# Kernel optimization log

Hardware: AMD Instinct MI355X
Metric: run time of the kernel (lower is better)

## Reference

```python
import jax, jax.numpy as jnp
import numpy as np


def setup_inputs() -> dict:
    key = jax.random.key(0)
    k1, k2, k3, k4, k5 = jax.random.split(key, 5)
    d_in, d_out, r = 1024, 1024, 32
    x = jax.random.normal(k1, (8, 8192, d_in), dtype=jnp.float32)
    W = jax.random.normal(k2, (d_out, d_in), dtype=jnp.float32) * (1.0 / np.sqrt(d_in))
    b = jax.random.normal(k3, (d_out,), dtype=jnp.float32) * 0.01
    V_r = jax.random.normal(k4, (d_in, r), dtype=jnp.float32) * (1.0 / np.sqrt(d_in))
    C = jax.random.normal(k5, (d_out, r), dtype=jnp.float32) * (1.0 / np.sqrt(r))
    return {"x": x, "W": W, "b": b, "V_r": V_r, "C": C}


def reference(x, W, b, V_r, C):
    # base = x @ W.T + b  (the quantized linear, modeled in fp32)
    base = jnp.einsum('bsd,od->bso', x, W) + b
    # low-rank correction: (x @ V_r) @ C.T  -- keep factored form, never
    # materialize the dense d_in x d_out correction matrix
    correction = jnp.einsum('bsr,or->bso', jnp.einsum('bsd,dr->bsr', x, V_r), C)
    return base + correction
```

## Files before the change

kernel.cpp:

```cpp
#include <hip/hip_runtime.h>
#include <hip/hip_bf16.h>

typedef __bf16 bf16_t;
typedef __bf16 bf16x8 __attribute__((ext_vector_type(8)));
typedef float  f32x4  __attribute__((ext_vector_type(4)));

#define DK 1024
#define DN 1024
#define RNK 32
#define BM 128
#define BN 256
#define BK 32
#define NKT 32

__global__ void weff_kernel(const float* __restrict__ W,
                            const float* __restrict__ Vr,
                            const float* __restrict__ C,
                            bf16_t* __restrict__ WeffSw)
{
    const int o  = blockIdx.x;
    const int g  = threadIdx.x;
    const int d0 = g * 8;

    f32x4 cv[8];
#pragma unroll
    for (int q = 0; q < 8; ++q) cv[q] = *(const f32x4*)(C + o * RNK + q * 4);

    const f32x4* wrow = (const f32x4*)(W + (size_t)o * DK + d0);
    f32x4 w0 = wrow[0], w1 = wrow[1];
    float acc[8];
#pragma unroll
    for (int e = 0; e < 4; ++e) { acc[e] = w0[e]; acc[4 + e] = w1[e]; }

#pragma unroll
    for (int e = 0; e < 8; ++e) {
        const f32x4* vre = (const f32x4*)(Vr + (size_t)(d0 + e) * RNK);
        float s = 0.f;
#pragma unroll
        for (int q = 0; q < 8; ++q) {
            f32x4 v = vre[q];
            s += cv[q][0] * v[0] + cv[q][1] * v[1] + cv[q][2] * v[2] + cv[q][3] * v[3];
        }
        acc[e] += s;
    }

    bf16x8 out;
#pragma unroll
    for (int e = 0; e < 8; ++e) out[e] = (bf16_t)acc[e];

    const int bn = o >> 8, rloc = o & 255;
    const int kt = d0 >> 5, seg = (d0 >> 3) & 3;
    const int sw = seg ^ ((rloc >> 1) & 3);
    const size_t byte = (size_t)(bn * 32 + kt) * 16384 + rloc * 64 + (sw << 4);
    *(bf16x8*)((char*)WeffSw + byte) = out;
}

__global__ __launch_bounds__(512, 4) void corrlin_gemm_kernel(
    const float* __restrict__ X, const bf16_t* __restrict__ WeffSw,
    const float* __restrict__ bias, float* __restrict__ Out)
{
    __shared__ __align__(16) char smem[49152];
    char* Ab0 = smem;
    char* Ab1 = smem + 8192;
    char* Bb0 = smem + 16384;
    char* Bb1 = smem + 32768;

    const int tid = threadIdx.x;
    const int nwg = gridDim.x;
    const int b0  = blockIdx.x;
    const int L   = (b0 & 7) * (nwg >> 3) + (b0 >> 3);
    const int bm  = L >> 2;
    const int bn  = L & 3;
    const int m0  = bm * BM;

    const int lane = tid & 63;
    const int wid  = tid >> 6;
    const int wm   = wid >> 2;
    const int wn   = wid & 3;
    const int arow = tid >> 2;
    const int aseg = tid & 3;

    f32x4 acc[4][4] = {};
    f32x4 set0[2], set1[2];

    auto issueA = [&](int kt, f32x4* s) {
        const float* p = X + (size_t)(m0 + arow) * DK + kt * BK + aseg * 8;
        s[0] = *(const f32x4*)p;
        s[1] = *(const f32x4*)(p + 4);
    };
    auto storeA = [&](const f32x4* s, char* Ab) {
        const int sw = aseg ^ ((arow >> 1) & 3);
        bf16x8 v;
#pragma unroll
        for (int j = 0; j < 4; ++j) { v[j] = (bf16_t)s[0][j]; v[4 + j] = (bf16_t)s[1][j]; }
        *(bf16x8*)(Ab + arow * 64 + (sw << 4)) = v;
    };
    auto issueB = [&](int kt, char* Bb) {
        const char* g = (const char*)WeffSw + (size_t)(bn * 32 + kt) * 16384;
#pragma unroll
        for (int c = 0; c < 2; ++c) {
            const int lin = wid * 2048 + c * 1024;
            __builtin_amdgcn_global_load_lds(
                (const __attribute__((address_space(1))) void*)(g + lin + lane * 16),
                (__attribute__((address_space(3))) void*)(Bb + lin),
                16, 0, 0);
        }
    };
    auto readB = [&](const char* Bc, bf16x8* bfr) {
        const int kb = lane >> 4;
#pragma unroll
        for (int nf = 0; nf < 4; ++nf) {
            const int row = wn * 64 + nf * 16 + (lane & 15);
            bfr[nf] = *(const bf16x8*)(Bc + row * 64 + ((kb ^ ((row >> 1) & 3)) << 4));
        }
    };
    auto compute = [&](const char* Ac, const bf16x8* bfr) {
        bf16x8 af[4];
        const int kb = lane >> 4;
#pragma unroll
        for (int i = 0; i < 4; ++i) {
            const int row = wm * 64 + i * 16 + (lane & 15);
            af[i] = *(const bf16x8*)(Ac + row * 64 + ((kb ^ ((row >> 1) & 3)) << 4));
        }
        __builtin_amdgcn_s_setprio(1);
#pragma unroll
        for (int mf = 0; mf < 4; ++mf)
#pragma unroll
            for (int nf = 0; nf < 4; ++nf)
                acc[mf][nf] = __builtin_amdgcn_mfma_f32_16x16x32_bf16(
                    af[mf], bfr[nf], acc[mf][nf], 0, 0, 0);
        __builtin_amdgcn_s_setprio(0);
    };

    auto iter = [&](int t, const char* Ac, const char* Bc, char* An, char* Bn,
                    f32x4* aStore , f32x4* aFill ) {
        if (t + 1 < NKT) issueB(t + 1, Bn);
        bf16x8 bfr[4];
        readB(Bc, bfr);
        if (t + 1 < NKT) storeA(aStore, An);
        if (t + 2 < NKT) issueA(t + 2, aFill);
        compute(Ac, bfr);
        if (t + 2 < NKT) {
            asm volatile("s_waitcnt vmcnt(2) lgkmcnt(0)" ::: "memory");
            __builtin_amdgcn_s_barrier();
        } else if (t + 1 < NKT) {
            asm volatile("s_waitcnt vmcnt(0) lgkmcnt(0)" ::: "memory");
            __builtin_amdgcn_s_barrier();
        }
    };

    issueA(0, set0);
    issueB(0, Bb0);
    storeA(set0, Ab0);
    issueA(1, set1);
    asm volatile("s_waitcnt vmcnt(2) lgkmcnt(0)" ::: "memory");
    __builtin_amdgcn_s_barrier();

    for (int t = 0; t < NKT; t += 2) {
        iter(t,     Ab0, Bb0, Ab1, Bb1, set1, set0);
        iter(t + 1, Ab1, Bb1, Ab0, Bb0, set0, set1);
    }
    __syncthreads();

    float* tb = (float*)smem + wid * 1280;
    const int mbase = m0 + wm * 64;
    const int nbase = bn * BN + wn * 64;
    float bv[4];
#pragma unroll
    for (int nf = 0; nf < 4; ++nf) bv[nf] = bias[nbase + nf * 16 + (lane & 15)];

#pragma unroll
    for (int mf = 0; mf < 4; ++mf) {
#pragma unroll
        for (int nf = 0; nf < 4; ++nf)
#pragma unroll
            for (int j = 0; j < 4; ++j) {
                const int r = (lane >> 4) * 4 + j;
                const int c = nf * 16 + (lane & 15);
                tb[r * 80 + c] = acc[mf][nf][j] + bv[nf];
            }
        __syncthreads();
#pragma unroll
        for (int jj = 0; jj < 4; ++jj) {
            const int rr = jj * 4 + (lane >> 4);
            const int cc = (lane & 15) * 4;
            f32x4 v = *(const f32x4*)&tb[rr * 80 + cc];
            *(f32x4*)&Out[(size_t)(mbase + mf * 16 + rr) * DN + nbase + cc] = v;
        }
        __syncthreads();
    }
}

extern "C" void kernel_launch(void* const* d_in, const int* in_sizes, int n_in,
                              void* d_out, int out_size, void* d_ws, size_t ws_size,
                              hipStream_t stream) {
    const float* x  = (const float*)d_in[0];
    const float* W  = (const float*)d_in[1];
    const float* b  = (const float*)d_in[2];
    const float* Vr = (const float*)d_in[3];
    const float* C  = (const float*)d_in[4];
    float* out = (float*)d_out;

    const int M = in_sizes[0] / DK;
    bf16_t* WeffSw = (bf16_t*)d_ws;

    weff_kernel<<<DN, 128, 0, stream>>>(W, Vr, C, WeffSw);

    const int mtiles = M / BM;
    const int nwg = mtiles * (DN / BN);
    corrlin_gemm_kernel<<<nwg, 512, 0, stream>>>(x, WeffSw, b, out);
}
```

Measured before the change: 229.1 us.

## Load B fragments directly from global in MFMA order, bypassing LDS

The folded weight matrix is now written by the prep kernel in a fragment-major layout, so each wave can load its MFMA B operands straight from global memory into registers with coalesced 16-byte loads. This removes the LDS staging buffers for B and the LDS reads used to fetch them, and shrinks shared memory. Register pressure rises from the double-buffered B fragments, so launch bounds drop from 4 to 2 blocks per CU. Each wave now fetches its own B slice from L2 instead of sharing it through LDS, which raises global traffic.

Measured after the change: 333.4 us. +45.5%, slower.

```diff
diff --git a/kernel.cpp b/kernel.cpp
--- a/kernel.cpp
+++ b/kernel.cpp
@@ -16,7 +16,7 @@
 __global__ void weff_kernel(const float* __restrict__ W,
                             const float* __restrict__ Vr,
                             const float* __restrict__ C,
-                            bf16_t* __restrict__ WeffSw)
+                            bf16_t* __restrict__ WeffF)
 {
     const int o  = blockIdx.x;
     const int g  = threadIdx.x;
@@ -48,22 +48,19 @@
 #pragma unroll
     for (int e = 0; e < 8; ++e) out[e] = (bf16_t)acc[e];
 
-    const int bn = o >> 8, rloc = o & 255;
-    const int kt = d0 >> 5, seg = (d0 >> 3) & 3;
-    const int sw = seg ^ ((rloc >> 1) & 3);
-    const size_t byte = (size_t)(bn * 32 + kt) * 16384 + rloc * 64 + (sw << 4);
-    *(bf16x8*)((char*)WeffSw + byte) = out;
+    const int n16 = o >> 4, r = o & 15;
+    const int k32 = d0 >> 5, kk = (d0 >> 3) & 3;
+    const size_t byte = (size_t)((n16 * 32 + k32) * 64 + r + kk * 16) * 16;
+    *(bf16x8*)((char*)WeffF + byte) = out;
 }
 
-__global__ __launch_bounds__(512, 4) void corrlin_gemm_kernel(
-    const float* __restrict__ X, const bf16_t* __restrict__ WeffSw,
+__global__ __launch_bounds__(512, 2) void corrlin_gemm_kernel(
+    const float* __restrict__ X, const bf16_t* __restrict__ WeffF,
     const float* __restrict__ bias, float* __restrict__ Out)
 {
-    __shared__ __align__(16) char smem[49152];
+    __shared__ __align__(16) char smem[40960];
     char* Ab0 = smem;
     char* Ab1 = smem + 8192;
-    char* Bb0 = smem + 16384;
-    char* Bb1 = smem + 32768;
 
     const int tid = threadIdx.x;
     const int nwg = gridDim.x;
@@ -82,6 +79,10 @@
 
     f32x4 acc[4][4] = {};
     f32x4 set0[2], set1[2];
+    bf16x8 bA[4], bB[4];
+
+    const char* WB = (const char*)WeffF;
+    const int nfrag0 = (bn * 16 + wn * 4) * 32;
 
     auto issueA = [&](int kt, f32x4* s) {
         const float* p = X + (size_t)(m0 + arow) * DK + kt * BK + aseg * 8;
@@ -95,24 +96,10 @@
         for (int j = 0; j < 4; ++j) { v[j] = (bf16_t)s[0][j]; v[4 + j] = (bf16_t)s[1][j]; }
         *(bf16x8*)(Ab + arow * 64 + (sw << 4)) = v;
     };
-    auto issueB = [&](int kt, char* Bb) {
-        const char* g = (const char*)WeffSw + (size_t)(bn * 32 + kt) * 16384;
+    auto loadB = [&](int kt, bf16x8* dst) {
 #pragma unroll
-        for (int c = 0; c < 2; ++c) {
-            const int lin = wid * 2048 + c * 1024;
-            __builtin_amdgcn_global_load_lds(
-                (const __attribute__((address_space(1))) void*)(g + lin + lane * 16),
-                (__attribute__((address_space(3))) void*)(Bb + lin),
-                16, 0, 0);
-        }
-    };
-    auto readB = [&](const char* Bc, bf16x8* bfr) {
-        const int kb = lane >> 4;
-#pragma unroll
-        for (int nf = 0; nf < 4; ++nf) {
-            const int row = wn * 64 + nf * 16 + (lane & 15);
-            bfr[nf] = *(const bf16x8*)(Bc + row * 64 + ((kb ^ ((row >> 1) & 3)) << 4));
-        }
+        for (int nf = 0; nf < 4; ++nf)
+            dst[nf] = *(const bf16x8*)(WB + (size_t)(nfrag0 + nf * 32 + kt) * 1024 + lane * 16);
     };
     auto compute = [&](const char* Ac, const bf16x8* bfr) {
         bf16x8 af[4];
@@ -132,33 +119,26 @@
         __builtin_amdgcn_s_setprio(0);
     };
 
-    auto iter = [&](int t, const char* Ac, const char* Bc, char* An, char* Bn,
+    auto iter = [&](int t, const char* Ac, char* An, const bf16x8* bCur, bf16x8* bNext,
                     f32x4* aStore , f32x4* aFill ) {
-        if (t + 1 < NKT) issueB(t + 1, Bn);
-        bf16x8 bfr[4];
-        readB(Bc, bfr);
+        if (t + 1 < NKT) loadB(t + 1, bNext);
         if (t + 1 < NKT) storeA(aStore, An);
         if (t + 2 < NKT) issueA(t + 2, aFill);
-        compute(Ac, bfr);
-        if (t + 2 < NKT) {
-            asm volatile("s_waitcnt vmcnt(2) lgkmcnt(0)" ::: "memory");
-            __builtin_amdgcn_s_barrier();
-        } else if (t + 1 < NKT) {
-            asm volatile("s_waitcnt vmcnt(0) lgkmcnt(0)" ::: "memory");
-            __builtin_amdgcn_s_barrier();
-        }
+        compute(Ac, bCur);
+        asm volatile("s_waitcnt lgkmcnt(0)" ::: "memory");
+        __builtin_amdgcn_s_barrier();
     };
 
     issueA(0, set0);
-    issueB(0, Bb0);
+    loadB(0, bA);
     storeA(set0, Ab0);
     issueA(1, set1);
-    asm volatile("s_waitcnt vmcnt(2) lgkmcnt(0)" ::: "memory");
+    asm volatile("s_waitcnt lgkmcnt(0)" ::: "memory");
     __builtin_amdgcn_s_barrier();
 
     for (int t = 0; t < NKT; t += 2) {
-        iter(t,     Ab0, Bb0, Ab1, Bb1, set1, set0);
-        iter(t + 1, Ab1, Bb1, Ab0, Bb0, set0, set1);
+        iter(t,     Ab0, Ab1, bA, bB, set1, set0);
+        iter(t + 1, Ab1, Ab0, bB, bA, set0, set1);
     }
     __syncthreads();
 
@@ -202,11 +182,11 @@
     float* out = (float*)d_out;
 
     const int M = in_sizes[0] / DK;
-    bf16_t* WeffSw = (bf16_t*)d_ws;
+    bf16_t* WeffF = (bf16_t*)d_ws;
 
-    weff_kernel<<<DN, 128, 0, stream>>>(W, Vr, C, WeffSw);
+    weff_kernel<<<DN, 128, 0, stream>>>(W, Vr, C, WeffF);
 
     const int mtiles = M / BM;
     const int nwg = mtiles * (DN / BN);
-    corrlin_gemm_kernel<<<nwg, 512, 0, stream>>>(x, WeffSw, b, out);
+    corrlin_gemm_kernel<<<nwg, 512, 0, stream>>>(x, WeffF, b, out);
 }
```
